# Kernel optimization log

Measured on AMD Instinct MI355X. Metric: run time of the kernel, lower is better.

Reference implementation:

```python
import jax, jax.numpy as jnp
import numpy as np

EPS = 1e-5
N_NODES = 100000
N_EDGES = 1600000
IN_F, HID_F, OUT_F = 128, 128, 64


def setup_inputs() -> dict:
    key = jax.random.key(0)
    ks = jax.random.split(key, 8)
    def xavier(k, fan_in, fan_out):
        lim = float(np.sqrt(6.0 / (fan_in + fan_out)))
        return jax.random.uniform(k, (fan_in, fan_out), jnp.float32, -lim, lim)
    return {
        "features": jax.random.normal(ks[0], (N_NODES, IN_F), jnp.float32),
        "src": jax.random.randint(ks[1], (N_EDGES,), 0, N_NODES, jnp.int64 if jax.config.jax_enable_x64 else jnp.int32),
        "dst": jax.random.randint(ks[2], (N_EDGES,), 0, N_NODES, jnp.int64 if jax.config.jax_enable_x64 else jnp.int32),
        "W_self1": xavier(ks[3], IN_F, HID_F),
        "W_neigh1": xavier(ks[4], IN_F, HID_F),
        "b1": jnp.zeros((HID_F,), jnp.float32),
        "gamma1": jnp.ones((HID_F,), jnp.float32),
        "beta1": jnp.zeros((HID_F,), jnp.float32),
        "W_self2": xavier(ks[5], HID_F, OUT_F),
        "W_neigh2": xavier(ks[6], HID_F, OUT_F),
        "b2": jnp.zeros((OUT_F,), jnp.float32),
        "gamma2": jnp.ones((OUT_F,), jnp.float32),
        "beta2": jnp.zeros((OUT_F,), jnp.float32),
    }


def _sage_conv(h, src, dst, W_self, W_neigh, b, n_nodes):
    # mean aggregation of source-node features onto destination nodes
    agg = jax.ops.segment_sum(h[src], dst, num_segments=n_nodes)   # [N, d]
    deg = jax.ops.segment_sum(jnp.ones_like(dst, dtype=h.dtype), dst, num_segments=n_nodes)
    h_neigh = agg / jnp.maximum(deg, 1.0)[:, None]                  # zero-degree -> 0
    return h @ W_self + h_neigh @ W_neigh + b


def _batchnorm(h, gamma, beta):
    # training-mode BatchNorm1d: batch stats over node dim, biased variance
    mu = jnp.mean(h, axis=0)
    var = jnp.mean(jnp.square(h - mu), axis=0)
    return (h - mu) * jax.lax.rsqrt(var + EPS) * gamma + beta


def reference(features, src, dst, W_self1, W_neigh1, b1, gamma1, beta1,
              W_self2, W_neigh2, b2, gamma2, beta2):
    n = features.shape[0]
    h = _sage_conv(features, src, dst, W_self1, W_neigh1, b1, n)
    h = jax.nn.relu(_batchnorm(h, gamma1, beta1))
    h = _sage_conv(h, src, dst, W_self2, W_neigh2, b2, n)
    return _batchnorm(h, gamma2, beta2)
```

## Files before the change

kernel.cpp:

```cpp
#include <hip/hip_runtime.h>

#define EPS_BN 1e-5f
#define BINSHIFT 9
#define BINW 512
#define P_EPB 8192
#define LDS_CAP 10240
#define NREP 32

typedef __attribute__((ext_vector_type(8))) short short8;
typedef __attribute__((ext_vector_type(4))) float f32x4;

__device__ __forceinline__ unsigned short f2bf(float x) {
    unsigned int u = __float_as_uint(x);
    u += 0x7fffu + ((u >> 16) & 1u);
    return (unsigned short)(u >> 16);
}
__device__ __forceinline__ float bf2f(unsigned short h) {
    return __uint_as_float(((unsigned int)h) << 16);
}
__device__ __forceinline__ float bflo(unsigned u) { return __uint_as_float(u << 16); }
__device__ __forceinline__ float bfhi(unsigned u) { return __uint_as_float(u & 0xffff0000u); }
__device__ __forceinline__ float i8lo(unsigned short u) { return (float)(signed char)(u & 0xff); }
__device__ __forceinline__ float i8hi(unsigned short u) { return (float)(signed char)(u >> 8); }

__device__ __forceinline__ void scan512(int* a, int t) {
    for (int off = 1; off < 512; off <<= 1) {
        int v = (t >= off) ? a[t - off] : 0;
        __syncthreads();
        a[t] += v;
        __syncthreads();
    }
}
__device__ __forceinline__ void scan256(int* a, int t) {
    for (int off = 1; off < 256; off <<= 1) {
        int v = (t >= off) ? a[t - off] : 0;
        __syncthreads();
        a[t] += v;
        __syncthreads();
    }
}

__global__ __launch_bounds__(256) void prep_kernel(
    const float* __restrict__ Ws1, const float* __restrict__ Wn1,
    const float* __restrict__ Ws2, const float* __restrict__ Wn2,
    unsigned short* __restrict__ W1f, unsigned short* __restrict__ W2f,
    const int* __restrict__ dst, int* __restrict__ counts, int E, int NB, int wB) {
    int tid = threadIdx.x;
    if (blockIdx.x < wB) {
        int i = blockIdx.x * 256 + tid;
        if (i < 128 * 256) {
            int j = i & 7, L = (i >> 3) & 63, c = (i >> 9) & 15, kk = i >> 13;
            int k = kk * 32 + (L >> 4) * 8 + j;
            int col = c * 16 + (L & 15);
            float v = (col < 128) ? Ws1[k * 128 + col] : Wn1[k * 128 + (col - 128)];
            W1f[i] = f2bf(v);
        } else {
            int idx = i - 128 * 256;
            if (idx < 128 * 128) {
                int j = idx & 7, L = (idx >> 3) & 63, c = (idx >> 9) & 7, kk = idx >> 12;
                int k = kk * 32 + (L >> 4) * 8 + j;
                int col = c * 16 + (L & 15);
                float v = (col < 64) ? Ws2[k * 64 + col] : Wn2[k * 64 + (col - 64)];
                W2f[idx] = f2bf(v);
            }
        }
    } else {
        __shared__ int hist[512];
        int blk = blockIdx.x - wB;
        int e0 = blk * P_EPB, e1 = min(e0 + P_EPB, E);
        for (int b = tid; b < 512; b += 256) hist[b] = 0;
        __syncthreads();
        for (int e = e0 + tid; e < e1; e += 256) atomicAdd(&hist[dst[e] >> BINSHIFT], 1);
        __syncthreads();
        for (int b = tid; b < NB; b += 256) counts[blk * NB + b] = hist[b];
    }
}

__global__ __launch_bounds__(256) void p2a(const int* __restrict__ counts,
                                           int* __restrict__ segrel,
                                           int* __restrict__ tot, int NB, int NBLK) {
    __shared__ int s[256];
    int b = blockIdx.x, t = threadIdx.x;
    int v = (t < NBLK) ? counts[t * NB + b] : 0;
    s[t] = v;
    __syncthreads();
    scan256(s, t);
    if (t < NBLK) segrel[t * NB + b] = s[t] - v;
    if (t == 255) tot[b] = s[255];
}

__global__ __launch_bounds__(512) void p3_scatter(const int* __restrict__ src,
                                                  const int* __restrict__ dst,
                                                  const int* __restrict__ segrel,
                                                  const int* __restrict__ tot,
                                                  unsigned* __restrict__ epack,
                                                  int E, int NB) {
    __shared__ unsigned lp[P_EPB];
    __shared__ int hist[512];
    __shared__ int sBase[513];
    __shared__ int cursor[512];
    __shared__ int bbase[512];
    int t = threadIdx.x;
    int blk = blockIdx.x;
    int e0 = blk * P_EPB, e1 = min(e0 + P_EPB, E), m = e1 - e0;
    int tv = (t < NB) ? tot[t] : 0;
    bbase[t] = tv;
    __syncthreads();
    scan512(bbase, t);
    bbase[t] -= tv;
    hist[t] = 0;
    __syncthreads();
    for (int e = e0 + t; e < e1; e += 512) atomicAdd(&hist[dst[e] >> BINSHIFT], 1);
    __syncthreads();
    int h = hist[t];
    scan512(hist, t);
    int excl = hist[t] - h;
    sBase[t] = excl;
    cursor[t] = excl;
    if (t == 0) sBase[512] = m;
    __syncthreads();
    for (int e = e0 + t; e < e1; e += 512) {
        int d = dst[e];
        int pos = atomicAdd(&cursor[d >> BINSHIFT], 1);
        lp[pos] = ((unsigned)src[e] << BINSHIFT) | ((unsigned)d & (BINW - 1));
    }
    __syncthreads();
    for (int i = t; i < m; i += 512) {
        int lo = 0, hi = NB;
        while (hi - lo > 1) {
            int mid = (lo + hi) >> 1;
            if (sBase[mid] <= i) lo = mid; else hi = mid;
        }
        epack[bbase[lo] + segrel[blk * NB + lo] + (i - sBase[lo])] = lp[i];
    }
}

__global__ __launch_bounds__(512) void p4_csr(const unsigned* __restrict__ epack,
                                              const int* __restrict__ tot,
                                              int* __restrict__ row_start,
                                              int* __restrict__ cntg,
                                              float* __restrict__ inv_deg,
                                              int* __restrict__ csr_src, int N, int NB) {
    __shared__ int ncnt[512];
    __shared__ int cursor[512];
    __shared__ int bb[512];
    __shared__ int lsrc[LDS_CAP];
    int t = threadIdx.x;
    int b = blockIdx.x;
    int tv = (t < NB) ? tot[t] : 0;
    bb[t] = tv;
    __syncthreads();
    scan512(bb, t);
    int e1 = bb[b];
    int e0 = bb[b] - tot[b];
    int m = e1 - e0;
    int nbase = b << BINSHIFT;
    int nn = min(N - nbase, BINW);
    ncnt[t] = 0;
    __syncthreads();
    for (int i = e0 + t; i < e1; i += 512)
        atomicAdd(&ncnt[epack[i] & (BINW - 1)], 1);
    __syncthreads();
    int c = ncnt[t];
    scan512(ncnt, t);
    int excl = ncnt[t] - c;
    if (t < nn) {
        int node = nbase + t;
        row_start[node] = e0 + excl;
        cntg[node] = c;
        inv_deg[node] = 1.0f / fmaxf((float)c, 1.0f);
    }
    cursor[t] = excl;
    __syncthreads();
    for (int i = e0 + t; i < e1; i += 512) {
        unsigned v = epack[i];
        int pos = atomicAdd(&cursor[v & (BINW - 1)], 1);
        if (pos < LDS_CAP) lsrc[pos] = (int)(v >> BINSHIFT);
    }
    __syncthreads();
    int mm = min(m, LDS_CAP);
    for (int i = t; i < mm; i += 512) csr_src[e0 + i] = lsrc[i];
}

template <int MT, int MSELF, bool SELFBF, bool FUSEBN, bool AFP32>
__global__ __launch_bounds__(256) void gemm_dual(const unsigned short* __restrict__ Ab,
                                                 const float* __restrict__ Af,
                                                 const unsigned short* __restrict__ Wf,
                                                 float* __restrict__ YselfF,
                                                 unsigned short* __restrict__ YselfB,
                                                 signed char* __restrict__ Ynb8,
                                                 float* __restrict__ scl, int N,
                                                 const float* __restrict__ sums,
                                                 const float* __restrict__ gamma,
                                                 const float* __restrict__ beta,
                                                 float invN) {
    constexpr int K = 128;
    constexpr int NCT = MT / 16;
    constexpr int NCTW = NCT / 2;
    constexpr int KS = K / 32;
    constexpr int MNB = MT - MSELF;
    static_assert(MSELF * 2 == MT, "col-half split requires MSELF == MT/2");
    __shared__ float ssc[128], ssh[128];

    if constexpr (FUSEBN) {
        if (threadIdx.x < 128) {
            int c = threadIdx.x;
            float su = 0.f, sq = 0.f;
            for (int r = 0; r < NREP; r++) {
                su += sums[r * 256 + c];
                sq += sums[r * 256 + 128 + c];
            }
            float mu = su * invN;
            float var = sq * invN - mu * mu;
            float sc = gamma[c] * rsqrtf(var + EPS_BN);
            ssc[c] = sc;
            ssh[c] = beta[c] - mu * sc;
        }
        __syncthreads();
    }

    int wv = threadIdx.x >> 6, lane = threadIdx.x & 63;
    int ch = wv & 1;
    int rt = wv >> 1;
    int row0 = blockIdx.x * 64 + rt * 32;
    int m = lane & 15, quad = lane >> 4;

    short8 afrag[2][KS];
#pragma unroll
    for (int t = 0; t < 2; t++) {
        int arow = row0 + t * 16 + m;
        if (arow >= N) arow = N - 1;
#pragma unroll
        for (int kk = 0; kk < KS; kk++) {
            short8 raw;
            if (AFP32) {
                const float* ap = Af + (size_t)arow * K + quad * 8 + kk * 32;
                f32x4 a = *(const f32x4*)ap;
                f32x4 b = *(const f32x4*)(ap + 4);
#pragma unroll
                for (int j = 0; j < 4; j++) {
                    raw[j] = (short)f2bf(a[j]);
                    raw[4 + j] = (short)f2bf(b[j]);
                }
            } else {
                raw = *(const short8*)(Ab + (size_t)arow * K + quad * 8 + kk * 32);
            }
            if (FUSEBN) {
#pragma unroll
                for (int j = 0; j < 8; j++) {
                    int c = kk * 32 + quad * 8 + j;
                    float f = bf2f((unsigned short)raw[j]) * ssc[c] + ssh[c];
                    raw[j] = (short)f2bf(fmaxf(f, 0.f));
                }
            }
            afrag[t][kk] = raw;
        }
    }

    f32x4 acc[2][NCTW];
#pragma unroll
    for (int t = 0; t < 2; t++)
        for (int ci = 0; ci < NCTW; ci++)
            for (int j = 0; j < 4; j++) acc[t][ci][j] = 0.f;

    const short8* Bf = (const short8*)Wf;
    int cbase = ch * NCTW;
#pragma unroll
    for (int kk = 0; kk < KS; kk++) {
#pragma unroll
        for (int ci = 0; ci < NCTW; ci++) {
            short8 bfrag = Bf[(kk * NCT + cbase + ci) * 64 + lane];
#pragma unroll
            for (int t = 0; t < 2; t++)
                acc[t][ci] = __builtin_amdgcn_mfma_f32_16x16x32_bf16(afrag[t][kk], bfrag,
                                                                     acc[t][ci], 0, 0, 0);
        }
    }

    if (ch == 0) {
#pragma unroll
        for (int t = 0; t < 2; t++) {
#pragma unroll
            for (int ci = 0; ci < NCTW; ci++) {
                int colg = ci * 16 + m;
#pragma unroll
                for (int r = 0; r < 4; r++) {
                    int row = row0 + t * 16 + quad * 4 + r;
                    if (row < N) {
                        float v = acc[t][ci][r];
                        if (SELFBF)
                            YselfB[(size_t)row * MSELF + colg] = f2bf(v);
                        else
                            YselfF[(size_t)row * MSELF + colg] = v;
                    }
                }
            }
        }
    } else {
#pragma unroll
        for (int t = 0; t < 2; t++) {
#pragma unroll
            for (int r = 0; r < 4; r++) {
                float mx = 0.f;
#pragma unroll
                for (int ci = 0; ci < NCTW; ci++) mx = fmaxf(mx, fabsf(acc[t][ci][r]));
#pragma unroll
                for (int off = 1; off < 16; off <<= 1) mx = fmaxf(mx, __shfl_xor(mx, off));
                int row = row0 + t * 16 + quad * 4 + r;
                float qs = 127.0f / fmaxf(mx, 1e-30f);
                if (row < N) {
                    if (m == 0) scl[row] = mx * (1.0f / 127.0f);
#pragma unroll
                    for (int ci = 0; ci < NCTW; ci++) {
                        int colg = ci * 16 + m;
                        int q = __float2int_rn(acc[t][ci][r] * qs);
                        Ynb8[(size_t)row * MNB + colg] = (signed char)q;
                    }
                }
            }
        }
    }
}

__global__ __launch_bounds__(256) void agg_row128(const unsigned int* __restrict__ Sb,
                                                  const unsigned short* __restrict__ Tq,
                                                  const float* __restrict__ scl,
                                                  const int* __restrict__ row_start,
                                                  const int* __restrict__ cnt,
                                                  const float* __restrict__ inv_deg,
                                                  const int* __restrict__ csr_src,
                                                  const float* __restrict__ bias,
                                                  unsigned int* __restrict__ Out,
                                                  float* __restrict__ sums,
                                                  int N, int totalWaves) {
    int wv = threadIdx.x >> 6, lane = threadIdx.x & 63;
    int c = lane * 2;
    float bs0 = bias[c], bs1 = bias[c + 1];
    float S0 = 0.f, S1 = 0.f, Q0 = 0.f, Q1 = 0.f;

    int n = blockIdx.x * 4 + wv;
    int pStart = 0, pEc = 0, pIv = 0;
    float pInv = 0.f;
    if (n < N) {
        pStart = row_start[n];
        pEc = cnt[n];
        pInv = inv_deg[n];
        if (pEc > 0) pIv = csr_src[pStart + min(lane, min(pEc, 64) - 1)];
    }
    for (; n < N; n += totalWaves) {
        int start = pStart, ec = pEc, iv = pIv;
        float inv = pInv;
        unsigned su = Sb[(size_t)n * 64 + lane];
        int n2 = n + totalWaves;
        if (n2 < N) {
            pStart = row_start[n2];
            pEc = cnt[n2];
            pInv = inv_deg[n2];
            if (pEc > 0) pIv = csr_src[pStart + min(lane, min(pEc, 64) - 1)];
        }
        float a0 = 0.f, a1 = 0.f;
        for (int base = 0; base < ec; base += 64) {
            int ecc = min(ec - base, 64);
            if (base) iv = csr_src[start + base + min(lane, ecc - 1)];
            int e = 0;
            for (; e + 16 <= ecc; e += 16) {
                unsigned short u[16];
                float sc[16];
#pragma unroll
                for (int j = 0; j < 16; j++) {
                    int s = __builtin_amdgcn_readlane(iv, e + j);
                    u[j] = Tq[(size_t)s * 64 + lane];
                    sc[j] = scl[s];
                }
#pragma unroll
                for (int j = 0; j < 16; j++) {
                    a0 += sc[j] * i8lo(u[j]);
                    a1 += sc[j] * i8hi(u[j]);
                }
            }
            if (e + 8 <= ecc) {
                unsigned short u[8];
                float sc[8];
#pragma unroll
                for (int j = 0; j < 8; j++) {
                    int s = __builtin_amdgcn_readlane(iv, e + j);
                    u[j] = Tq[(size_t)s * 64 + lane];
                    sc[j] = scl[s];
                }
#pragma unroll
                for (int j = 0; j < 8; j++) {
                    a0 += sc[j] * i8lo(u[j]);
                    a1 += sc[j] * i8hi(u[j]);
                }
                e += 8;
            }
            if (e < ecc) {
                int r = ecc - e;
                unsigned short u[8];
                float sc[8];
#pragma unroll
                for (int j = 0; j < 8; j++) {
                    int s = __builtin_amdgcn_readlane(iv, min(e + j, ecc - 1));
                    u[j] = Tq[(size_t)s * 64 + lane];
                    sc[j] = scl[s];
                }
#pragma unroll
                for (int j = 0; j < 8; j++) {
                    if (j < r) {
                        a0 += sc[j] * i8lo(u[j]);
                        a1 += sc[j] * i8hi(u[j]);
                    }
                }
            }
        }
        float h0 = bflo(su) + a0 * inv + bs0;
        float h1 = bfhi(su) + a1 * inv + bs1;
        Out[(size_t)n * 64 + lane] = (unsigned)f2bf(h0) | ((unsigned)f2bf(h1) << 16);
        S0 += h0; Q0 += h0 * h0;
        S1 += h1; Q1 += h1 * h1;
    }
    __shared__ float ls[256];
    ls[threadIdx.x] = 0.f;
    __syncthreads();
    atomicAdd(&ls[c], S0);
    atomicAdd(&ls[c + 1], S1);
    atomicAdd(&ls[128 + c], Q0);
    atomicAdd(&ls[129 + c], Q1);
    __syncthreads();
    float* dstS = sums + (size_t)(blockIdx.x & (NREP - 1)) * 256;
    atomicAdd(&dstS[threadIdx.x], ls[threadIdx.x]);
}

__global__ __launch_bounds__(256) void agg_row64(const unsigned short* __restrict__ Tq,
                                                 const float* __restrict__ scl,
                                                 const int* __restrict__ row_start,
                                                 const int* __restrict__ cnt,
                                                 const float* __restrict__ inv_deg,
                                                 const int* __restrict__ csr_src,
                                                 const float* __restrict__ bias,
                                                 float* Self, float* __restrict__ sums,
                                                 int N, int totalWaves) {
    int wv = threadIdx.x >> 6, lane = threadIdx.x & 63;
    int g = lane >> 5, h = lane & 31;
    int c = h * 2;
    float bs0 = bias[c], bs1 = bias[c + 1];
    float S0 = 0.f, S1 = 0.f, Q0 = 0.f, Q1 = 0.f;

    int n = blockIdx.x * 4 + wv;
    int pStart = 0, pEc = 0, pIv = 0;
    if (n < N) {
        pStart = row_start[n];
        pEc = cnt[n];
        if (pEc > 0) pIv = csr_src[pStart + min(lane, min(pEc, 64) - 1)];
    }
    for (; n < N; n += totalWaves) {
        int start = pStart, ec = pEc, iv = pIv;
        float inv = inv_deg[n];
        int n2 = n + totalWaves;
        if (n2 < N) {
            pStart = row_start[n2];
            pEc = cnt[n2];
            if (pEc > 0) pIv = csr_src[pStart + min(lane, min(pEc, 64) - 1)];
        }
        float a0 = 0.f, a1 = 0.f;
        for (int base = 0; base < ec; base += 64) {
            int ecc = min(ec - base, 64);
            if (base) iv = csr_src[start + base + min(lane, ecc - 1)];
            int e = 0;
            for (; e + 8 <= ecc; e += 8) {
                unsigned short u[4];
                float sc[4];
#pragma unroll
                for (int j = 0; j < 4; j++) {
                    int s0 = __builtin_amdgcn_readlane(iv, e + 2 * j);
                    int s1 = __builtin_amdgcn_readlane(iv, e + 2 * j + 1);
                    int sg = g ? s1 : s0;
                    u[j] = Tq[(size_t)sg * 32 + h];
                    sc[j] = scl[sg];
                }
#pragma unroll
                for (int j = 0; j < 4; j++) {
                    a0 += sc[j] * i8lo(u[j]);
                    a1 += sc[j] * i8hi(u[j]);
                }
            }
            if (e < ecc) {
                int r = ecc - e;
                unsigned short u[4];
                float sc[4];
#pragma unroll
                for (int j = 0; j < 4; j++) {
                    int s0 = __builtin_amdgcn_readlane(iv, min(e + 2 * j, ecc - 1));
                    int s1 = __builtin_amdgcn_readlane(iv, min(e + 2 * j + 1, ecc - 1));
                    int sg = g ? s1 : s0;
                    u[j] = Tq[(size_t)sg * 32 + h];
                    sc[j] = scl[sg];
                }
#pragma unroll
                for (int j = 0; j < 4; j++) {
                    bool ok = (2 * j + g) < r;
                    a0 += ok ? sc[j] * i8lo(u[j]) : 0.f;
                    a1 += ok ? sc[j] * i8hi(u[j]) : 0.f;
                }
            }
        }
        a0 += __shfl_xor(a0, 32);
        a1 += __shfl_xor(a1, 32);
        if (g == 0) {
            size_t off = (size_t)n * 64 + c;
            float h0 = Self[off] + a0 * inv + bs0;
            float h1 = Self[off + 1] + a1 * inv + bs1;
            Self[off] = h0;
            Self[off + 1] = h1;
            S0 += h0; Q0 += h0 * h0;
            S1 += h1; Q1 += h1 * h1;
        }
    }
    __shared__ float ls[128];
    if (threadIdx.x < 128) ls[threadIdx.x] = 0.f;
    __syncthreads();
    if (g == 0) {
        atomicAdd(&ls[c], S0);
        atomicAdd(&ls[c + 1], S1);
        atomicAdd(&ls[64 + c], Q0);
        atomicAdd(&ls[65 + c], Q1);
    }
    __syncthreads();
    if (threadIdx.x < 128) {
        float* dstS = sums + (size_t)(blockIdx.x & (NREP - 1)) * 128;
        atomicAdd(&dstS[threadIdx.x], ls[threadIdx.x]);
    }
}

__global__ __launch_bounds__(256) void bn_apply_f64(float* H, const float* __restrict__ sums,
                                                    const float* __restrict__ gamma,
                                                    const float* __restrict__ beta,
                                                    int N, float invN) {
    __shared__ float ss[128];
    int tid = threadIdx.x;
    if (tid < 64) {
        float su = 0.f, sq = 0.f;
        for (int r = 0; r < NREP; r++) {
            su += sums[r * 128 + tid];
            sq += sums[r * 128 + 64 + tid];
        }
        float mu = su * invN;
        float var = sq * invN - mu * mu;
        float sc = gamma[tid] * rsqrtf(var + EPS_BN);
        ss[tid] = sc;
        ss[64 + tid] = beta[tid] - mu * sc;
    }
    __syncthreads();
    int total4 = N * 16;
    float4* H4 = (float4*)H;
    for (int i = blockIdx.x * 256 + threadIdx.x; i < total4; i += 256 * gridDim.x) {
        int c0 = (i * 4) & 63;
        float4 v = H4[i];
        float4 sc = *(const float4*)&ss[c0];
        float4 sh = *(const float4*)&ss[64 + c0];
        v.x = v.x * sc.x + sh.x;
        v.y = v.y * sc.y + sh.y;
        v.z = v.z * sc.z + sh.z;
        v.w = v.w * sc.w + sh.w;
        H4[i] = v;
    }
}

extern "C" void kernel_launch(void* const* d_in, const int* in_sizes, int n_in,
                              void* d_out, int out_size, void* d_ws, size_t ws_size,
                              hipStream_t stream) {
    const float* X = (const float*)d_in[0];
    const int* src = (const int*)d_in[1];
    const int* dst = (const int*)d_in[2];
    const float* Wself1 = (const float*)d_in[3];
    const float* Wneigh1 = (const float*)d_in[4];
    const float* b1 = (const float*)d_in[5];
    const float* g1 = (const float*)d_in[6];
    const float* be1 = (const float*)d_in[7];
    const float* Wself2 = (const float*)d_in[8];
    const float* Wneigh2 = (const float*)d_in[9];
    const float* b2 = (const float*)d_in[10];
    const float* g2 = (const float*)d_in[11];
    const float* be2 = (const float*)d_in[12];
    float* out = (float*)d_out;

    const int N = in_sizes[0] / 128;
    const int E = in_sizes[1];
    const int NB = (N + BINW - 1) >> BINSHIFT;
    const int NBLK = (E + P_EPB - 1) / P_EPB;

    char* p = (char*)d_ws;
    auto carve = [&](size_t bytes) {
        char* r = p;
        p += (bytes + 255) & ~(size_t)255;
        return r;
    };
    float* sums1 = (float*)carve((size_t)NREP * 256 * 4);
    float* sums2 = (float*)carve((size_t)NREP * 128 * 4);
    size_t zero_bytes = (size_t)(p - (char*)d_ws);
    int* counts = (int*)carve((size_t)NBLK * NB * 4);
    int* segrel = (int*)carve((size_t)NBLK * NB * 4);
    int* tot = (int*)carve((size_t)NB * 4);
    unsigned* epack = (unsigned*)carve((size_t)E * 4);
    int* csr_src = (int*)carve((size_t)E * 4);
    int* row_start = (int*)carve((size_t)N * 4);
    int* cntg = (int*)carve((size_t)N * 4);
    float* inv_deg = (float*)carve((size_t)N * 4);
    unsigned short* W1f = (unsigned short*)carve(128 * 256 * 2);
    unsigned short* W2f = (unsigned short*)carve(128 * 128 * 2);
    unsigned short* bufS = (unsigned short*)carve((size_t)N * 128 * 2);
    signed char* Tq1 = (signed char*)carve((size_t)N * 128);
    float* scl1 = (float*)carve((size_t)N * 4);
    signed char* Tq2 = (signed char*)carve((size_t)N * 64);
    float* scl2 = (float*)carve((size_t)N * 4);
    unsigned short* h1b = (unsigned short*)carve((size_t)N * 128 * 2);

    hipMemsetAsync(d_ws, 0, zero_bytes, stream);

    const int wB = 192;
    const float invN = 1.0f / (float)N;
    prep_kernel<<<wB + NBLK, 256, 0, stream>>>(Wself1, Wneigh1, Wself2, Wneigh2, W1f, W2f,
                                               dst, counts, E, NB, wB);
    p2a<<<NB, 256, 0, stream>>>(counts, segrel, tot, NB, NBLK);
    p3_scatter<<<NBLK, 512, 0, stream>>>(src, dst, segrel, tot, epack, E, NB);
    p4_csr<<<NB, 512, 0, stream>>>(epack, tot, row_start, cntg, inv_deg, csr_src, N, NB);

    int ggrid = (N + 63) / 64;
    gemm_dual<256, 128, true, false, true><<<ggrid, 256, 0, stream>>>(
        nullptr, X, W1f, nullptr, bufS, Tq1, scl1, N, nullptr, nullptr, nullptr, 0.f);
    agg_row128<<<2048, 256, 0, stream>>>(
        (const unsigned int*)bufS, (const unsigned short*)Tq1, scl1, row_start, cntg,
        inv_deg, csr_src, b1, (unsigned int*)h1b, sums1, N, 8192);

    gemm_dual<128, 64, false, true, false><<<ggrid, 256, 0, stream>>>(
        h1b, nullptr, W2f, out, nullptr, Tq2, scl2, N, sums1, g1, be1, invN);
    agg_row64<<<2048, 256, 0, stream>>>(
        (const unsigned short*)Tq2, scl2, row_start, cntg, inv_deg, csr_src, b2, out,
        sums2, N, 8192);
    bn_apply_f64<<<2048, 256, 0, stream>>>(out, sums2, g2, be2, N, invN);
}
```

Baseline: 338.3 us.

## Scatter edges directly to global and stage GEMM A tiles through padded LDS

The edge scatter kernel drops its LDS local sort (histogram, scan, binary-search copy-out) and writes packed edges straight to global memory using per-bin cursors initialised from the global bases plus per-block offsets. This removes a pass and several barriers, at the cost of scattered uncoalesced global writes. The dual GEMM kernel now loads its 64-row A tile cooperatively into padded shared memory with coalesced vector loads and reads fragments from LDS. This avoids duplicate, strided global reads across the column-half warps, but adds LDS usage and may lower occupancy.

After: 315.0 us. 6.9% less time.

```diff
diff --git a/kernel.cpp b/kernel.cpp
--- a/kernel.cpp
+++ b/kernel.cpp
@@ -95,43 +95,22 @@
                                                   const int* __restrict__ tot,
                                                   unsigned* __restrict__ epack,
                                                   int E, int NB) {
-    __shared__ unsigned lp[P_EPB];
-    __shared__ int hist[512];
-    __shared__ int sBase[513];
-    __shared__ int cursor[512];
-    __shared__ int bbase[512];
+    __shared__ int cur[512];
     int t = threadIdx.x;
     int blk = blockIdx.x;
-    int e0 = blk * P_EPB, e1 = min(e0 + P_EPB, E), m = e1 - e0;
+    int e0 = blk * P_EPB, e1 = min(e0 + P_EPB, E);
     int tv = (t < NB) ? tot[t] : 0;
-    bbase[t] = tv;
-    __syncthreads();
-    scan512(bbase, t);
-    bbase[t] -= tv;
-    hist[t] = 0;
-    __syncthreads();
-    for (int e = e0 + t; e < e1; e += 512) atomicAdd(&hist[dst[e] >> BINSHIFT], 1);
-    __syncthreads();
-    int h = hist[t];
-    scan512(hist, t);
-    int excl = hist[t] - h;
-    sBase[t] = excl;
-    cursor[t] = excl;
-    if (t == 0) sBase[512] = m;
+    cur[t] = tv;
+    __syncthreads();
+    scan512(cur, t);
+    int base = cur[t] - tv;
+    __syncthreads();
+    cur[t] = (t < NB) ? (base + segrel[blk * NB + t]) : 0;
     __syncthreads();
     for (int e = e0 + t; e < e1; e += 512) {
         int d = dst[e];
-        int pos = atomicAdd(&cursor[d >> BINSHIFT], 1);
-        lp[pos] = ((unsigned)src[e] << BINSHIFT) | ((unsigned)d & (BINW - 1));
-    }
-    __syncthreads();
-    for (int i = t; i < m; i += 512) {
-        int lo = 0, hi = NB;
-        while (hi - lo > 1) {
-            int mid = (lo + hi) >> 1;
-            if (sBase[mid] <= i) lo = mid; else hi = mid;
-        }
-        epack[bbase[lo] + segrel[blk * NB + lo] + (i - sBase[lo])] = lp[i];
+        int pos = atomicAdd(&cur[d >> BINSHIFT], 1);
+        epack[pos] = ((unsigned)src[e] << BINSHIFT) | ((unsigned)d & (BINW - 1));
     }
 }
 
@@ -199,8 +178,11 @@
     constexpr int NCTW = NCT / 2;
     constexpr int KS = K / 32;
     constexpr int MNB = MT - MSELF;
+    constexpr int APADF = 132;
+    constexpr int APADH = 136;
     static_assert(MSELF * 2 == MT, "col-half split requires MSELF == MT/2");
     __shared__ float ssc[128], ssh[128];
+    __shared__ __align__(16) char AsRaw[AFP32 ? (64 * APADF * 4) : (64 * APADH * 2)];
 
     if constexpr (FUSEBN) {
         if (threadIdx.x < 128) {
@@ -216,25 +198,43 @@
             ssc[c] = sc;
             ssh[c] = beta[c] - mu * sc;
         }
-        __syncthreads();
-    }
+    }
+
+    int row0g = blockIdx.x * 64;
+    if (AFP32) {
+        float* As = (float*)AsRaw;
+        for (int i = threadIdx.x; i < 64 * 32; i += 256) {
+            int r = i >> 5, cv = i & 31;
+            int gr = row0g + r;
+            if (gr >= N) gr = N - 1;
+            *(f32x4*)&As[r * APADF + cv * 4] = *(const f32x4*)&Af[(size_t)gr * K + cv * 4];
+        }
+    } else {
+        unsigned short* As = (unsigned short*)AsRaw;
+        for (int i = threadIdx.x; i < 64 * 16; i += 256) {
+            int r = i >> 4, cv = i & 15;
+            int gr = row0g + r;
+            if (gr >= N) gr = N - 1;
+            *(short8*)&As[r * APADH + cv * 8] = *(const short8*)&Ab[(size_t)gr * K + cv * 8];
+        }
+    }
+    __syncthreads();
 
     int wv = threadIdx.x >> 6, lane = threadIdx.x & 63;
     int ch = wv & 1;
     int rt = wv >> 1;
-    int row0 = blockIdx.x * 64 + rt * 32;
+    int row0 = row0g + rt * 32;
     int m = lane & 15, quad = lane >> 4;
 
     short8 afrag[2][KS];
 #pragma unroll
     for (int t = 0; t < 2; t++) {
-        int arow = row0 + t * 16 + m;
-        if (arow >= N) arow = N - 1;
+        int lr = rt * 32 + t * 16 + m;
 #pragma unroll
         for (int kk = 0; kk < KS; kk++) {
             short8 raw;
             if (AFP32) {
-                const float* ap = Af + (size_t)arow * K + quad * 8 + kk * 32;
+                const float* ap = ((const float*)AsRaw) + lr * APADF + quad * 8 + kk * 32;
                 f32x4 a = *(const f32x4*)ap;
                 f32x4 b = *(const f32x4*)(ap + 4);
 #pragma unroll
@@ -243,7 +243,8 @@
                     raw[4 + j] = (short)f2bf(b[j]);
                 }
             } else {
-                raw = *(const short8*)(Ab + (size_t)arow * K + quad * 8 + kk * 32);
+                raw = *(const short8*)(((const unsigned short*)AsRaw) + lr * APADH +
+                                       quad * 8 + kk * 32);
             }
             if (FUSEBN) {
 #pragma unroll
```
